# Performance work log

Hardware: AMD Instinct MI355X
Metric: run time of the kernel (lower is better)

The kernel has to match this reference:

```python
import jax, jax.numpy as jnp
import numpy as np

# Module dims (match init_kwargs / input_specs)
V = 25        # number of graph nodes (chain skeleton)
K = 3         # max receptive-field size (neighbors incl. self), padded
CIN = 64
COUT = 64
N = 16
T = 512
TK = 3        # temporal_kernel
PAD = TK // 2 # time_pad default


def _build_graph():
    # Chain adjacency with self-links: node i <-> {i-1, i, i+1}
    A = np.zeros((V, V), np.float32)
    for i in range(V):
        A[i, i] = 1.0
        if i > 0:
            A[i, i - 1] = 1.0
        if i < V - 1:
            A[i, i + 1] = 1.0
    # Pad each node's neighbor list to K entries; mask marks real neighbors.
    idx = np.zeros((V, K), np.int32)
    mask = np.zeros((V, K), bool)
    for i in range(V):
        nb = np.where(A[i] != 0)[0]
        idx[i, : len(nb)] = nb
        mask[i, : len(nb)] = True
    return idx, mask


def setup_inputs() -> dict:
    key = jax.random.key(0)
    k_x, k_w, k_b = jax.random.split(key, 3)
    x = jax.random.normal(k_x, (N, CIN, V, T), dtype=jnp.float32)
    # One Conv2d kernel per node: [V, C_out, C_in, K, TK]; padded neighbor
    # slots are zeroed via mask inside reference().
    W = jax.random.normal(k_w, (V, COUT, CIN, K, TK), dtype=jnp.float32) * 0.05
    b = jax.random.normal(k_b, (V, COUT), dtype=jnp.float32) * 0.05
    idx_np, mask_np = _build_graph()
    return {
        "x": x,
        "W": W,
        "b": b,
        "idx": jnp.asarray(idx_np),
        "mask": jnp.asarray(mask_np),
    }


def reference(x, W, b, idx, mask):
    # x: [N, C, V, T]; W: [V, O, C, K, TK]; b: [V, O]; idx/mask: [V, K]
    Tt = x.shape[-1]
    # Zero out padded neighbor slots so padded rows contribute nothing
    # (equivalent to torch's variable-height per-node kernels).
    Wm = jnp.where(mask[:, None, None, :, None], W, 0.0)
    # Temporal zero padding (Conv2d padding=(0, time_pad))
    xp = jnp.pad(x, ((0, 0), (0, 0), (0, 0), (PAD, PAD)))
    # Batched neighbor gather: [N, C, V, K, T + 2*PAD]
    g = xp[:, :, idx, :]
    # Cross-correlation over the TK temporal taps (stride 1)
    out = jnp.zeros((x.shape[0], W.shape[1], V, Tt), dtype=x.dtype)
    for kt in range(TK):
        out = out + jnp.einsum(
            "ncvkt,vock->novt", g[..., kt : kt + Tt], Wm[..., kt]
        )
    out = out + b.T[None, :, :, None]  # per-node bias [O, V]
    return out
```

## Files before the change

### kernel.cpp

```cpp
#include <hip/hip_runtime.h>
#include <hip/hip_bf16.h>

#define NB   16
#define CINC 64
#define COUTC 64
#define NV   25
#define TLEN 512
#define KK   3
#define TKK  3

typedef short short8 __attribute__((ext_vector_type(8)));
typedef float f32x4  __attribute__((ext_vector_type(4)));
typedef float f32x16 __attribute__((ext_vector_type(16)));

#define XS_STRIDE 17408
#define NWT3BLK (NV * 9)

__device__ __forceinline__ unsigned pack_bf16(float lo, float hi) {
  __hip_bfloat16 l = __float2bfloat16(lo);
  __hip_bfloat16 h = __float2bfloat16(hi);
  unsigned short ul = *reinterpret_cast<unsigned short*>(&l);
  unsigned short uh = *reinterpret_cast<unsigned short*>(&h);
  return (unsigned)ul | ((unsigned)uh << 16);
}

__global__ __launch_bounds__(256) void prep_all(
    const float* __restrict__ x, const float* __restrict__ W,
    const unsigned char* __restrict__ mask_raw,
    __hip_bfloat16* __restrict__ Wt3, __hip_bfloat16* __restrict__ xT) {
  __shared__ float ts[64][65];
  int bid = blockIdx.x;
  if (bid < NWT3BLK) {
    int blk = bid;
    int v = blk / 9, kkt = blk % 9, k = kkt / 3, kt = kkt % 3;
    const int* mi = (const int*)mask_raw;
    int ok = 1;
    for (int i = 0; i < 18; ++i) {
      int m = mi[i];
      if (m != 0 && m != 1) ok = 0;
    }
    int m = ok ? mi[v * KK + k] : (int)(mask_raw[v * KK + k] != 0);
    const float* Wv = W + (size_t)v * COUTC * CINC * 9;
    __hip_bfloat16* dst = Wt3 + (size_t)blk * 4096;
    for (int i = threadIdx.x; i < 4096; i += 256) {
      int e     = i & 7;
      int lane  = (i >> 3) & 63;
      int ks    = (i >> 9) & 3;
      int oslab = i >> 11;
      int o = oslab * 32 + (lane & 31);
      int c = ks * 16 + 8 * (lane >> 5) + e;
      float val = m ? Wv[(o * CINC + c) * 9 + k * 3 + kt] : 0.f;
      dst[i] = __float2bfloat16(val);
    }
    return;
  }
  bid -= NWT3BLK;
  const int tb = (bid & 7) * 64;
  const int vn = bid >> 3;
  const int v  = vn % NV;
  const int n  = vn / NV;
  const int tid = threadIdx.x;
  for (int i = tid; i < 1024; i += 256) {
    int c = i >> 4, tq = (i & 15) * 4;
    float4 val = *(const float4*)(x + (((size_t)n * CINC + c) * NV + v) * TLEN + tb + tq);
    ts[c][tq + 0] = val.x;
    ts[c][tq + 1] = val.y;
    ts[c][tq + 2] = val.z;
    ts[c][tq + 3] = val.w;
  }
  __syncthreads();
  unsigned* dst = (unsigned*)(xT + (((size_t)n * NV + v) * TLEN + tb) * CINC);
  for (int i = tid; i < 2048; i += 256) {
    int c2 = i & 31, t = i >> 5;
    dst[t * 32 + c2] = pack_bf16(ts[2 * c2][t], ts[2 * c2 + 1][t]);
  }
}

__device__ __forceinline__ const char* slab_base(const __hip_bfloat16* xT,
                                                 int n, int vk, int tb) {
  return (const char*)xT + ((ptrdiff_t)((n * NV + vk) * TLEN + tb) - 1) * 128;
}

__device__ __forceinline__ void stage_slab(const char* gbase, char* lbase,
                                           int wave, int lane) {
  for (int c = wave; c < 17; c += 4) {
    int L = c * 1024 + lane * 16;
    int g = L ^ (((L >> 7) & 7) << 4);
    __builtin_amdgcn_global_load_lds(
        (const __attribute__((address_space(1))) void*)(gbase + g),
        (__attribute__((address_space(3))) void*)(lbase + c * 1024),
        16, 0, 0);
  }
}

__device__ __forceinline__ void fix_edges(char* buf, int tb, int tid) {
  if (tb == 0 && tid < 8)
    *(f32x4*)(buf + tid * 16) = (f32x4){0.f, 0.f, 0.f, 0.f};
  if (tb == TLEN - 128 && tid >= 8 && tid < 16)
    *(f32x4*)(buf + 129 * 128 + (tid - 8) * 16) = (f32x4){0.f, 0.f, 0.f, 0.f};
}

__global__ __launch_bounds__(256, 2) void lcn_mfma32(
    const __hip_bfloat16* __restrict__ xT,
    const __hip_bfloat16* __restrict__ Wt3,
    const float* __restrict__ bias,
    const int* __restrict__ idx,
    float* __restrict__ out) {
  __shared__ char xs[2][XS_STRIDE];

  const int tb   = blockIdx.x * 128;
  const int v    = blockIdx.y;
  const int n    = blockIdx.z;
  const int tid  = threadIdx.x;
  const int lane = tid & 63;
  const int wave = tid >> 6;
  const int wt   = wave * 32;
  const int hi   = lane >> 5;
  const int l31  = lane & 31;

  f32x16 acc0 = {};
  f32x16 acc1 = {};

  stage_slab(slab_base(xT, n, idx[v * KK + 0], tb), xs[0], wave, lane);
  __syncthreads();
  fix_edges(xs[0], tb, tid);
  __syncthreads();

  const short8* wbase = (const short8*)Wt3;

  for (int k = 0; k < KK; ++k) {
    char* cur = xs[k & 1];
    char* nxt = xs[(k & 1) ^ 1];

    short8 a[2][3][4];
    const int blk0 = (v * KK + k) * TKK;
#pragma unroll
    for (int os = 0; os < 2; ++os)
#pragma unroll
      for (int kt = 0; kt < TKK; ++kt) {
        const short8* p = wbase + (((blk0 + kt) * 2 + os) << 8) + lane;
#pragma unroll
        for (int ks = 0; ks < 4; ++ks) a[os][kt][ks] = p[ks << 6];
      }

    if (k < KK - 1)
      stage_slab(slab_base(xT, n, idx[v * KK + k + 1], tb), nxt, wave, lane);

#pragma unroll
    for (int kt = 0; kt < TKK; ++kt) {
      const int r  = wt + l31 + kt;
      const char* bp = cur + r * 128;
      const int sw = (r & 7) << 4;
      const int co = hi * 16;
#pragma unroll
      for (int ks = 0; ks < 4; ++ks) {
        short8 b = *(const short8*)(bp + ((co + 32 * ks) ^ sw));
        acc0 = __builtin_amdgcn_mfma_f32_32x32x16_bf16(a[0][kt][ks], b, acc0, 0, 0, 0);
        acc1 = __builtin_amdgcn_mfma_f32_32x32x16_bf16(a[1][kt][ks], b, acc1, 0, 0, 0);
      }
    }

    __syncthreads();
    if (k < KK - 1) {
      fix_edges(nxt, tb, tid);
      __syncthreads();
    }
  }

  const float* bv = bias + v * COUTC;
  const int t = tb + wt + l31;
#pragma unroll
  for (int os = 0; os < 2; ++os) {
    const f32x16& acc = os ? acc1 : acc0;
#pragma unroll
    for (int reg = 0; reg < 16; ++reg) {
      int o = os * 32 + 4 * hi + (reg & 3) + 8 * (reg >> 2);
      out[(((size_t)n * COUTC + o) * NV + v) * TLEN + t] = acc[reg] + bv[o];
    }
  }
}

__global__ void prep_mask_kernel(const int* __restrict__ mask_raw,
                                 int* __restrict__ mask_out) {
  __shared__ int fmt;
  if (threadIdx.x == 0) {
    int ok = 1;
    for (int i = 0; i < 18; ++i) {
      int m = mask_raw[i];
      if (m != 0 && m != 1) ok = 0;
    }
    fmt = ok;
  }
  __syncthreads();
  int i = threadIdx.x;
  if (i < NV * KK) {
    int m;
    if (fmt) m = mask_raw[i];
    else     m = (((const unsigned char*)mask_raw)[i] != 0) ? 1 : 0;
    mask_out[i] = m;
  }
}

__global__ void prep_wt_kernel(const float* __restrict__ W,
                               float* __restrict__ Wt) {
  int v   = blockIdx.x / 9;
  int kkt = blockIdx.x % 9;
  const float* Wv = W + (size_t)v * COUTC * CINC * 9;
  float* dst = Wt + (size_t)blockIdx.x * (CINC * COUTC);
  for (int i = threadIdx.x; i < CINC * COUTC; i += 256) {
    int c = i >> 6;
    int o = i & 63;
    dst[i] = Wv[(o * CINC + c) * 9 + kkt];
  }
}

__global__ __launch_bounds__(256, 4) void lcn_main(
    const float* __restrict__ x, const float* __restrict__ Wt,
    const float* __restrict__ b, const int* __restrict__ idx,
    const int* __restrict__ maskn, float* __restrict__ out) {
  __shared__ float xsf[CINC][66];
  __shared__ float wsh[CINC][COUTC];
  const int tb  = blockIdx.x * 64;
  const int v   = blockIdx.y;
  const int n   = blockIdx.z;
  const int tid = threadIdx.x;
  const int t0  = tid & 63;
  const int og  = tid >> 6;
  float acc[16];
#pragma unroll
  for (int j = 0; j < 16; ++j) acc[j] = 0.f;
  for (int k = 0; k < KK; ++k) {
    const int vk = idx[v * KK + k];
    const int mk = maskn[v * KK + k];
    __syncthreads();
    for (int i = tid; i < CINC * 66; i += 256) {
      int c  = i / 66;
      int tt = i - c * 66;
      int gt = tb - 1 + tt;
      float val = 0.f;
      if (mk && gt >= 0 && gt < TLEN)
        val = x[(((size_t)n * CINC + c) * NV + vk) * TLEN + gt];
      xsf[c][tt] = val;
    }
    for (int kt = 0; kt < TKK; ++kt) {
      __syncthreads();
      const float4* src =
          (const float4*)(Wt + ((size_t)(v * KK + k) * TKK + kt) * (CINC * COUTC));
      for (int i = tid; i < CINC * COUTC / 4; i += 256)
        ((float4*)wsh)[i] = src[i];
      __syncthreads();
#pragma unroll 4
      for (int c = 0; c < CINC; ++c) {
        float xv = xsf[c][t0 + kt];
        const float4* wrow = (const float4*)&wsh[c][og * 16];
#pragma unroll
        for (int j4 = 0; j4 < 4; ++j4) {
          float4 wv = wrow[j4];
          acc[j4 * 4 + 0] = fmaf(wv.x, xv, acc[j4 * 4 + 0]);
          acc[j4 * 4 + 1] = fmaf(wv.y, xv, acc[j4 * 4 + 1]);
          acc[j4 * 4 + 2] = fmaf(wv.z, xv, acc[j4 * 4 + 2]);
          acc[j4 * 4 + 3] = fmaf(wv.w, xv, acc[j4 * 4 + 3]);
        }
      }
    }
  }
#pragma unroll
  for (int j = 0; j < 16; ++j) {
    int o = og * 16 + j;
    out[(((size_t)n * COUTC + o) * NV + v) * TLEN + tb + t0] =
        acc[j] + b[v * COUTC + o];
  }
}

extern "C" void kernel_launch(void* const* d_in, const int* in_sizes, int n_in,
                              void* d_out, int out_size, void* d_ws, size_t ws_size,
                              hipStream_t stream) {
  const float* x    = (const float*)d_in[0];
  const float* W    = (const float*)d_in[1];
  const float* b    = (const float*)d_in[2];
  const int*   idx  = (const int*)d_in[3];
  const void*  mask = (const void*)d_in[4];
  float* out = (float*)d_out;

  const size_t WT3_BYTES = (size_t)NV * 9 * 4096 * sizeof(__hip_bfloat16);
  const size_t XT_BYTES  = (size_t)NB * NV * TLEN * CINC * sizeof(__hip_bfloat16);
  const size_t NEED      = 512 + WT3_BYTES + XT_BYTES + 2048;

  if (ws_size >= NEED) {
    __hip_bfloat16* Wt3 = (__hip_bfloat16*)((char*)d_ws + 512);
    __hip_bfloat16* xT  = (__hip_bfloat16*)((char*)d_ws + 512 + WT3_BYTES);
    hipLaunchKernelGGL(prep_all, dim3(NWT3BLK + 8 * NV * NB), dim3(256), 0,
                       stream, x, W, (const unsigned char*)mask, Wt3, xT);
    hipLaunchKernelGGL(lcn_mfma32, dim3(TLEN / 128, NV, NB), dim3(256), 0,
                       stream, xT, Wt3, b, idx, out);
  } else {
    int*   maskn = (int*)d_ws;
    float* Wt    = (float*)((char*)d_ws + 512);
    hipLaunchKernelGGL(prep_mask_kernel, dim3(1), dim3(128), 0, stream,
                       (const int*)mask, maskn);
    hipLaunchKernelGGL(prep_wt_kernel, dim3(NV * KK * TKK), dim3(256), 0, stream,
                       W, Wt);
    hipLaunchKernelGGL(lcn_main, dim3(TLEN / 64, NV, NB), dim3(256), 0, stream,
                       x, Wt, b, idx, maskn, out);
  }
}
```

Baseline: 54.62 us.

## Process two batch samples per block and pre-pad xT to drop edge fixups

Result: faster. 52.88 us (-3.2%).

```diff
diff --git a/kernel.cpp b/kernel.cpp
--- a/kernel.cpp
+++ b/kernel.cpp
@@ -13,7 +13,8 @@
 typedef float f32x4  __attribute__((ext_vector_type(4)));
 typedef float f32x16 __attribute__((ext_vector_type(16)));
 
-#define XS_STRIDE 17408
+#define XT_ROWS 514
+#define XS_BYTES 16640
 #define NWT3BLK (NV * 9)
 
 __device__ __forceinline__ unsigned pack_bf16(float lo, float hi) {
@@ -69,35 +70,32 @@
     ts[c][tq + 3] = val.w;
   }
   __syncthreads();
-  unsigned* dst = (unsigned*)(xT + (((size_t)n * NV + v) * TLEN + tb) * CINC);
+  unsigned* base = (unsigned*)(xT + ((size_t)(n * NV + v) * XT_ROWS) * CINC);
   for (int i = tid; i < 2048; i += 256) {
     int c2 = i & 31, t = i >> 5;
-    dst[t * 32 + c2] = pack_bf16(ts[2 * c2][t], ts[2 * c2 + 1][t]);
-  }
+    base[(tb + 1 + t) * 32 + c2] = pack_bf16(ts[2 * c2][t], ts[2 * c2 + 1][t]);
+  }
+  if (tb == 0 && tid < 32) base[tid] = 0u;
+  if (tb == TLEN - 64 && tid < 32) base[513 * 32 + tid] = 0u;
 }
 
 __device__ __forceinline__ const char* slab_base(const __hip_bfloat16* xT,
                                                  int n, int vk, int tb) {
-  return (const char*)xT + ((ptrdiff_t)((n * NV + vk) * TLEN + tb) - 1) * 128;
+  return (const char*)xT + ((size_t)(n * NV + vk) * XT_ROWS + tb) * 128;
 }
 
 __device__ __forceinline__ void stage_slab(const char* gbase, char* lbase,
                                            int wave, int lane) {
   for (int c = wave; c < 17; c += 4) {
     int L = c * 1024 + lane * 16;
-    int g = L ^ (((L >> 7) & 7) << 4);
-    __builtin_amdgcn_global_load_lds(
-        (const __attribute__((address_space(1))) void*)(gbase + g),
-        (__attribute__((address_space(3))) void*)(lbase + c * 1024),
-        16, 0, 0);
-  }
-}
-
-__device__ __forceinline__ void fix_edges(char* buf, int tb, int tid) {
-  if (tb == 0 && tid < 8)
-    *(f32x4*)(buf + tid * 16) = (f32x4){0.f, 0.f, 0.f, 0.f};
-  if (tb == TLEN - 128 && tid >= 8 && tid < 16)
-    *(f32x4*)(buf + 129 * 128 + (tid - 8) * 16) = (f32x4){0.f, 0.f, 0.f, 0.f};
+    if (L < XS_BYTES) {
+      int g = L ^ (((L >> 7) & 7) << 4);
+      __builtin_amdgcn_global_load_lds(
+          (const __attribute__((address_space(1))) void*)(gbase + g),
+          (__attribute__((address_space(3))) void*)(lbase + c * 1024),
+          16, 0, 0);
+    }
+  }
 }
 
 __global__ __launch_bounds__(256, 2) void lcn_mfma32(
@@ -106,11 +104,12 @@
     const float* __restrict__ bias,
     const int* __restrict__ idx,
     float* __restrict__ out) {
-  __shared__ char xs[2][XS_STRIDE];
+  __shared__ char xs[2][2][XS_BYTES];
 
   const int tb   = blockIdx.x * 128;
-  const int v    = blockIdx.y;
-  const int n    = blockIdx.z;
+  const int np   = blockIdx.y;
+  const int v    = blockIdx.z;
+  const int n0   = np * 2;
   const int tid  = threadIdx.x;
   const int lane = tid & 63;
   const int wave = tid >> 6;
@@ -118,21 +117,36 @@
   const int hi   = lane >> 5;
   const int l31  = lane & 31;
 
-  f32x16 acc0 = {};
-  f32x16 acc1 = {};
-
-  stage_slab(slab_base(xT, n, idx[v * KK + 0], tb), xs[0], wave, lane);
-  __syncthreads();
-  fix_edges(xs[0], tb, tid);
-  __syncthreads();
+  f32x16 acc00 = {}, acc01 = {};
+  f32x16 acc10 = {}, acc11 = {};
+
+  {
+    const int vk0 = idx[v * KK + 0];
+    stage_slab(slab_base(xT, n0, vk0, tb),     xs[0][0], wave, lane);
+    stage_slab(slab_base(xT, n0 + 1, vk0, tb), xs[0][1], wave, lane);
+  }
 
   const short8* wbase = (const short8*)Wt3;
 
+#define COMPUTE_SLAB(BUF, ACC0, ACC1)                                          \
+  _Pragma("unroll")                                                            \
+  for (int kt = 0; kt < TKK; ++kt) {                                           \
+    const int r = wt + l31 + kt;                                               \
+    const char* bp = (BUF) + r * 128;                                          \
+    const int sw = (r & 7) << 4;                                               \
+    const int co = hi * 16;                                                    \
+    _Pragma("unroll")                                                          \
+    for (int ks = 0; ks < 4; ++ks) {                                           \
+      short8 bfr = *(const short8*)(bp + ((co + 32 * ks) ^ sw));               \
+      ACC0 = __builtin_amdgcn_mfma_f32_32x32x16_bf16(a[0][kt][ks], bfr, ACC0,  \
+                                                     0, 0, 0);                 \
+      ACC1 = __builtin_amdgcn_mfma_f32_32x32x16_bf16(a[1][kt][ks], bfr, ACC1,  \
+                                                     0, 0, 0);                 \
+    }                                                                          \
+  }
+
   for (int k = 0; k < KK; ++k) {
-    char* cur = xs[k & 1];
-    char* nxt = xs[(k & 1) ^ 1];
-
-    short8 a[2][3][4];
+    short8 a[2][TKK][4];
     const int blk0 = (v * KK + k) * TKK;
 #pragma unroll
     for (int os = 0; os < 2; ++os)
@@ -143,39 +157,36 @@
         for (int ks = 0; ks < 4; ++ks) a[os][kt][ks] = p[ks << 6];
       }
 
-    if (k < KK - 1)
-      stage_slab(slab_base(xT, n, idx[v * KK + k + 1], tb), nxt, wave, lane);
-
-#pragma unroll
-    for (int kt = 0; kt < TKK; ++kt) {
-      const int r  = wt + l31 + kt;
-      const char* bp = cur + r * 128;
-      const int sw = (r & 7) << 4;
-      const int co = hi * 16;
-#pragma unroll
-      for (int ks = 0; ks < 4; ++ks) {
-        short8 b = *(const short8*)(bp + ((co + 32 * ks) ^ sw));
-        acc0 = __builtin_amdgcn_mfma_f32_32x32x16_bf16(a[0][kt][ks], b, acc0, 0, 0, 0);
-        acc1 = __builtin_amdgcn_mfma_f32_32x32x16_bf16(a[1][kt][ks], b, acc1, 0, 0, 0);
-      }
-    }
-
     __syncthreads();
+
     if (k < KK - 1) {
-      fix_edges(nxt, tb, tid);
-      __syncthreads();
-    }
-  }
+      const int vk1 = idx[v * KK + k + 1];
+      char* nbuf0 = xs[(k + 1) & 1][0];
+      char* nbuf1 = xs[(k + 1) & 1][1];
+      stage_slab(slab_base(xT, n0, vk1, tb),     nbuf0, wave, lane);
+      stage_slab(slab_base(xT, n0 + 1, vk1, tb), nbuf1, wave, lane);
+    }
+
+    const char* cb0 = xs[k & 1][0];
+    const char* cb1 = xs[k & 1][1];
+    COMPUTE_SLAB(cb0, acc00, acc01)
+    COMPUTE_SLAB(cb1, acc10, acc11)
+  }
+#undef COMPUTE_SLAB
 
   const float* bv = bias + v * COUTC;
   const int t = tb + wt + l31;
 #pragma unroll
-  for (int os = 0; os < 2; ++os) {
-    const f32x16& acc = os ? acc1 : acc0;
-#pragma unroll
-    for (int reg = 0; reg < 16; ++reg) {
-      int o = os * 32 + 4 * hi + (reg & 3) + 8 * (reg >> 2);
-      out[(((size_t)n * COUTC + o) * NV + v) * TLEN + t] = acc[reg] + bv[o];
+  for (int nn = 0; nn < 2; ++nn) {
+#pragma unroll
+    for (int os = 0; os < 2; ++os) {
+      const f32x16& acc = nn ? (os ? acc11 : acc10) : (os ? acc01 : acc00);
+#pragma unroll
+      for (int reg = 0; reg < 16; ++reg) {
+        int o = os * 32 + 4 * hi + (reg & 3) + 8 * (reg >> 2);
+        out[(((size_t)(n0 + nn) * COUTC + o) * NV + v) * TLEN + t] =
+            acc[reg] + bv[o];
+      }
     }
   }
 }
@@ -283,7 +294,7 @@
   float* out = (float*)d_out;
 
   const size_t WT3_BYTES = (size_t)NV * 9 * 4096 * sizeof(__hip_bfloat16);
-  const size_t XT_BYTES  = (size_t)NB * NV * TLEN * CINC * sizeof(__hip_bfloat16);
+  const size_t XT_BYTES  = (size_t)NB * NV * XT_ROWS * CINC * sizeof(__hip_bfloat16);
   const size_t NEED      = 512 + WT3_BYTES + XT_BYTES + 2048;
 
   if (ws_size >= NEED) {
@@ -291,7 +302,7 @@
     __hip_bfloat16* xT  = (__hip_bfloat16*)((char*)d_ws + 512 + WT3_BYTES);
     hipLaunchKernelGGL(prep_all, dim3(NWT3BLK + 8 * NV * NB), dim3(256), 0,
                        stream, x, W, (const unsigned char*)mask, Wt3, xT);
-    hipLaunchKernelGGL(lcn_mfma32, dim3(TLEN / 128, NV, NB), dim3(256), 0,
+    hipLaunchKernelGGL(lcn_mfma32, dim3(TLEN / 128, NB / 2, NV), dim3(256), 0,
                        stream, xT, Wt3, b, idx, out);
   } else {
     int*   maskn = (int*)d_ws;
```
